# Kernel optimization log

Hardware: AMD Instinct MI355X
Metric: run time of the kernel (lower is better)

The kernel has to match this reference:

```python
import jax, jax.numpy as jnp
import numpy as np
from jax import lax

B, CI, CO, H, W, N, K = 16, 200, 128, 128, 128, 1024, 3
EPS = 1e-5


def setup_inputs() -> dict:
    key = jax.random.key(0)
    ks = jax.random.split(key, 23)
    rn = lambda i, s: jax.random.normal(ks[i], s, jnp.float32)
    ru = lambda i, s: jax.random.uniform(ks[i], s, jnp.float32)
    return {
        "X_in": rn(0, (B, CI, H, W)),
        "H_in": rn(1, (B, CI, N)),
        "bn1_gamma": ru(2, (CI,)),
        "bn1_beta": rn(3, (CI,)) * 0.1,
        "bn1_mean": rn(4, (CI,)) * 0.1,
        "bn1_var": ru(5, (CI,)) + 0.5,
        "bn2_gamma": ru(6, (CI,)),
        "bn2_beta": rn(7, (CI,)) * 0.1,
        "bn2_mean": rn(8, (CI,)) * 0.1,
        "bn2_var": ru(9, (CI,)) + 0.5,
        "W_lin": rn(10, (CO, CI)) * 0.05,
        "b_lin": rn(11, (CO,)) * 0.01,
        "W_sim": rn(12, (CO, CO)) * 0.05,
        "b_sim": rn(13, (CO,)) * 0.01,
        "W_score": rn(14, (CO, CO)) * 0.05,
        "b_score": rn(15, (CO,)) * 0.01,
        "W_dw": rn(16, (CO, 1, K, K)) * 0.1,
        "b_dw": rn(17, (CO,)) * 0.01,
        "W_final": rn(18, (CO, CI + CO)) * 0.05,
        "b_final": rn(19, (CO,)) * 0.01,
        "act_a": ru(20, (1,)),
        "act2_a": ru(21, (1,)),
        "final_a": ru(22, (1,)),
    }


def _bn(x, g, be, m, v):
    # BatchNorm1d eval: x [b,c,n]
    s = g / jnp.sqrt(v + EPS)
    return (x - m[None, :, None]) * s[None, :, None] + be[None, :, None]


def _c1(x, Wt, bi):
    # 1x1 Conv1d: x [b,c,n] -> [b,o,n]
    return jnp.einsum('oc,bcn->bon', Wt, x) + bi[None, :, None]


def _prelu(x, a):
    return jnp.where(x >= 0, x, a * x)


def reference(X_in, H_in, bn1_gamma, bn1_beta, bn1_mean, bn1_var,
              bn2_gamma, bn2_beta, bn2_mean, bn2_var,
              W_lin, b_lin, W_sim, b_sim, W_score, b_score,
              W_dw, b_dw, W_final, b_final, act_a, act2_a, final_a):
    b, c, h, w = X_in.shape
    n = H_in.shape[-1]
    Xr = X_in.reshape(b, c, h * w)
    X_bn = _bn(Xr, bn1_gamma, bn1_beta, bn1_mean, bn1_var)      # [b,ci,hw]
    H_bn = _bn(H_in, bn2_gamma, bn2_beta, bn2_mean, bn2_var)    # [b,ci,n]
    X = _c1(X_bn, W_lin, b_lin)                                  # [b,co,hw]
    Hn = _c1(H_bn, W_lin, b_lin)                                 # [b,co,n]
    X_mean = jnp.mean(X, axis=-1, keepdims=True)                 # [b,co,1]
    X_sim = _c1(X_mean, W_sim, b_sim)                            # [b,co,1]
    H_sim = _c1(Hn, W_sim, b_sim)                                # [b,co,n]
    H_sim2 = jnp.concatenate([X_sim, H_sim], axis=-1)            # [b,co,n+1]
    q = X_sim[:, :, 0]                                           # [b,co]
    sim = jax.nn.sigmoid(jnp.einsum('bc,bcn->bn', q, H_sim2))    # [b,n+1]
    sim = jax.nn.softmax(sim, axis=-1)
    vals = jnp.concatenate([X_mean, Hn], axis=-1)                # [b,co,n+1]
    X_aggre = jnp.einsum('bn,bcn->bc', sim, vals)                # [b,co]
    score = jax.nn.sigmoid(X_aggre @ W_score.T + b_score)        # [b,co]
    X4 = X.reshape(b, -1, h, w)
    Xdw = lax.conv_general_dilated(X4, W_dw, (1, 1), [(K // 2, K // 2)] * 2,
                                   feature_group_count=X4.shape[1],
                                   dimension_numbers=('NCHW', 'OIHW', 'NCHW'))
    Xdw = Xdw + b_dw[None, :, None, None]
    s4 = score[:, :, None, None]
    Xg = s4 * X_aggre[:, :, None, None] + (1.0 - s4) * Xdw       # gated blend
    Xg = _prelu(Xg, act_a)
    Hn = _prelu(Hn, act2_a)
    H_out = _prelu(_c1(jnp.concatenate([Hn, H_bn], axis=1), W_final, b_final), final_a)
    X_out = _prelu(_c1(jnp.concatenate([Xg.reshape(b, -1, h * w), X_bn], axis=1),
                       W_final, b_final), final_a)
    return X_out.reshape(b, -1, h, w), H_out
```

## Files before the change

### kernel.cpp

```cpp
#include <hip/hip_runtime.h>

constexpr int BB = 16;
constexpr int CI = 200;
constexpr int CO = 128;
constexpr int IMG_H = 128;
constexpr int IMG_W = 128;
constexpr int HW = IMG_H * IMG_W;
constexpr int NN = 1024;
constexpr int KT = CO + CI;

constexpr size_t OFF_X      = 0;
constexpr size_t OFF_HN     = (size_t)BB * CO * HW;
constexpr size_t OFF_WLIN1T = OFF_HN + (size_t)BB * CO * NN;
constexpr size_t OFF_WLIN2T = OFF_WLIN1T + (size_t)CI * CO;
constexpr size_t OFF_BLIN1  = OFF_WLIN2T + (size_t)CI * CO;
constexpr size_t OFF_BLIN2  = OFF_BLIN1 + CO;
constexpr size_t OFF_WCXT   = OFF_BLIN2 + CO;
constexpr size_t OFF_WCHT   = OFF_WCXT + (size_t)KT * CO;
constexpr size_t OFF_BFX    = OFF_WCHT + (size_t)KT * CO;
constexpr size_t OFF_BFH    = OFF_BFX + CO;
constexpr size_t OFF_XMSUM  = OFF_BFH + CO;
constexpr size_t OFF_GA     = OFF_XMSUM + (size_t)BB * CO;
constexpr size_t OFF_GB     = OFF_GA + (size_t)BB * CO;

__device__ __forceinline__ float preluf(float v, float a) { return v >= 0.f ? v : a * v; }

#define GEMM_FMA_8x8(wrow, xrow)                                        \
  {                                                                     \
    float4 a0 = *(const float4*)(wrow);                                 \
    float4 a1 = *(const float4*)((wrow) + 4);                           \
    float4 b0 = *(const float4*)(xrow);                                 \
    float4 b1 = *(const float4*)((xrow) + 4);                           \
    float av[8] = {a0.x, a0.y, a0.z, a0.w, a1.x, a1.y, a1.z, a1.w};     \
    float bv[8] = {b0.x, b0.y, b0.z, b0.w, b1.x, b1.y, b1.z, b1.w};     \
    _Pragma("unroll")                                                   \
    for (int ii = 0; ii < 8; ++ii)                                      \
      _Pragma("unroll")                                                 \
      for (int jj = 0; jj < 8; ++jj)                                    \
        acc[ii][jj] = fmaf(av[ii], bv[jj], acc[ii][jj]);                \
  }

__global__ __launch_bounds__(256) void k_prep(
    const float* __restrict__ bn1g, const float* __restrict__ bn1b,
    const float* __restrict__ bn1m, const float* __restrict__ bn1v,
    const float* __restrict__ bn2g, const float* __restrict__ bn2b,
    const float* __restrict__ bn2m, const float* __restrict__ bn2v,
    const float* __restrict__ Wlin, const float* __restrict__ blin,
    const float* __restrict__ Wfin, const float* __restrict__ bfin,
    float* ws)
{
  __shared__ float a1[CI], d1[CI], a2[CI], d2[CI];
  __shared__ float red[256];
  const int o = blockIdx.x;
  const int t = threadIdx.x;
  if (t < CI) {
    float s1 = bn1g[t] * rsqrtf(bn1v[t] + 1e-5f);
    a1[t] = s1; d1[t] = bn1b[t] - bn1m[t] * s1;
    float s2 = bn2g[t] * rsqrtf(bn2v[t] + 1e-5f);
    a2[t] = s2; d2[t] = bn2b[t] - bn2m[t] * s2;
  }
  __syncthreads();
  for (int k = t; k < CI; k += 256) {
    float w = Wlin[o * CI + k];
    ws[OFF_WLIN1T + (size_t)k * CO + o] = w * a1[k];
    ws[OFF_WLIN2T + (size_t)k * CO + o] = w * a2[k];
  }
  for (int k = t; k < KT; k += 256) {
    float w = Wfin[o * KT + k];
    float wx = w, wh = w;
    if (k >= CO) { wx = w * a1[k - CO]; wh = w * a2[k - CO]; }
    ws[OFF_WCXT + (size_t)k * CO + o] = wx;
    ws[OFF_WCHT + (size_t)k * CO + o] = wh;
  }
  if (t < BB) ws[OFF_XMSUM + (size_t)t * CO + o] = 0.f;

  float p1 = 0.f, p2 = 0.f, p3 = 0.f, p4 = 0.f;
  if (t < CI) {
    float wl = Wlin[o * CI + t];
    float wf = Wfin[o * KT + CO + t];
    p1 = wl * d1[t]; p2 = wl * d2[t];
    p3 = wf * d1[t]; p4 = wf * d2[t];
  }
  __syncthreads();
  red[t] = p1; __syncthreads();
  for (int s = 128; s > 0; s >>= 1) { if (t < s) red[t] += red[t + s]; __syncthreads(); }
  if (t == 0) ws[OFF_BLIN1 + o] = blin[o] + red[0];
  __syncthreads();
  red[t] = p2; __syncthreads();
  for (int s = 128; s > 0; s >>= 1) { if (t < s) red[t] += red[t + s]; __syncthreads(); }
  if (t == 0) ws[OFF_BLIN2 + o] = blin[o] + red[0];
  __syncthreads();
  red[t] = p3; __syncthreads();
  for (int s = 128; s > 0; s >>= 1) { if (t < s) red[t] += red[t + s]; __syncthreads(); }
  if (t == 0) ws[OFF_BFX + o] = bfin[o] + red[0];
  __syncthreads();
  red[t] = p4; __syncthreads();
  for (int s = 128; s > 0; s >>= 1) { if (t < s) red[t] += red[t + s]; __syncthreads(); }
  if (t == 0) ws[OFF_BFH + o] = bfin[o] + red[0];
}

__global__ __launch_bounds__(256) void k_hn(const float* __restrict__ Hin, float* ws)
{
  __shared__ __align__(16) float smem[2048];
  float* wt = smem;
  float* xb = smem + 1024;
  const float* WT = ws + OFF_WLIN2T;
  const float* bias = ws + OFF_BLIN2;
  float* Hn = ws + OFF_HN;
  const int bb = blockIdx.y;
  const int col0 = blockIdx.x * 128;
  const int tid = threadIdx.x;
  const int ty = tid >> 4, tx = tid & 15;
  const int kk = tid >> 5, j4 = tid & 31;
  float acc[8][8];
#pragma unroll
  for (int i = 0; i < 8; ++i)
#pragma unroll
    for (int j = 0; j < 8; ++j) acc[i][j] = 0.f;
  const float* Bsrc = Hin + (size_t)bb * CI * NN + col0;
  for (int k0 = 0; k0 < CI; k0 += 8) {
    ((float4*)wt)[tid] = ((const float4*)(WT + (size_t)(k0 + kk) * CO))[j4];
    ((float4*)xb)[tid] = ((const float4*)(Bsrc + (size_t)(k0 + kk) * NN))[j4];
    __syncthreads();
#pragma unroll
    for (int k = 0; k < 8; ++k) {
      const float* wrow = wt + k * 128 + ty * 8;
      const float* xrow = xb + k * 128 + tx * 8;
      GEMM_FMA_8x8(wrow, xrow);
    }
    __syncthreads();
  }
#pragma unroll
  for (int i = 0; i < 8; ++i) {
    const int o = ty * 8 + i;
    const float bi = bias[o];
    float* dst = Hn + ((size_t)(bb * CO + o)) * NN + col0 + tx * 8;
    *(float4*)dst       = make_float4(acc[i][0] + bi, acc[i][1] + bi, acc[i][2] + bi, acc[i][3] + bi);
    *(float4*)(dst + 4) = make_float4(acc[i][4] + bi, acc[i][5] + bi, acc[i][6] + bi, acc[i][7] + bi);
  }
}

__global__ __launch_bounds__(256) void k_x(const float* __restrict__ Xin, float* ws)
{
  __shared__ __align__(16) float smem[2048];
  float* wt = smem;
  float* xb = smem + 1024;
  const float* WT = ws + OFF_WLIN1T;
  const float* bias = ws + OFF_BLIN1;
  float* X = ws + OFF_X;
  const int bb = blockIdx.y;
  const int col0 = blockIdx.x * 128;
  const int tid = threadIdx.x;
  const int ty = tid >> 4, tx = tid & 15;
  const int kk = tid >> 5, j4 = tid & 31;
  float acc[8][8];
#pragma unroll
  for (int i = 0; i < 8; ++i)
#pragma unroll
    for (int j = 0; j < 8; ++j) acc[i][j] = 0.f;
  const float* Bsrc = Xin + (size_t)bb * CI * HW + col0;
  for (int k0 = 0; k0 < CI; k0 += 8) {
    ((float4*)wt)[tid] = ((const float4*)(WT + (size_t)(k0 + kk) * CO))[j4];
    ((float4*)xb)[tid] = ((const float4*)(Bsrc + (size_t)(k0 + kk) * HW))[j4];
    __syncthreads();
#pragma unroll
    for (int k = 0; k < 8; ++k) {
      const float* wrow = wt + k * 128 + ty * 8;
      const float* xrow = xb + k * 128 + tx * 8;
      GEMM_FMA_8x8(wrow, xrow);
    }
    __syncthreads();
  }
  float ps[8];
#pragma unroll
  for (int i = 0; i < 8; ++i) {
    const int o = ty * 8 + i;
    const float bi = bias[o];
    float s = 0.f;
#pragma unroll
    for (int j = 0; j < 8; ++j) s += acc[i][j];
    ps[i] = s;
    float* dst = X + ((size_t)(bb * CO + o)) * HW + col0 + tx * 8;
    *(float4*)dst       = make_float4(acc[i][0] + bi, acc[i][1] + bi, acc[i][2] + bi, acc[i][3] + bi);
    *(float4*)(dst + 4) = make_float4(acc[i][4] + bi, acc[i][5] + bi, acc[i][6] + bi, acc[i][7] + bi);
  }
  __syncthreads();
  float* red = smem;
#pragma unroll
  for (int i = 0; i < 8; ++i) red[(ty * 8 + i) * 16 + tx] = ps[i];
  __syncthreads();
  if (tid < 128) {
    float s = 0.f;
#pragma unroll
    for (int u = 0; u < 16; ++u) s += red[tid * 16 + u];
    atomicAdd(ws + OFF_XMSUM + (size_t)bb * CO + tid, s);
  }
}

__global__ __launch_bounds__(256) void k_small(
    const float* __restrict__ Wsim, const float* __restrict__ bsim,
    const float* __restrict__ Wscore, const float* __restrict__ bscore,
    float* ws)
{
  __shared__ float xmean[128], q[128], u[128], xa[128];
  __shared__ float sim[1025];
  __shared__ float red[256];
  __shared__ float cq_sh, l0_sh, msh, ssh;
  const int bb = blockIdx.x, t = threadIdx.x;
  const float* Hn = ws + OFF_HN + (size_t)bb * CO * NN;
  if (t < 128) xmean[t] = ws[OFF_XMSUM + (size_t)bb * CO + t] * (1.f / 16384.f) + ws[OFF_BLIN1 + t];
  __syncthreads();
  if (t < 128) {
    float s = bsim[t];
    for (int c = 0; c < 128; ++c) s = fmaf(Wsim[t * 128 + c], xmean[c], s);
    q[t] = s;
  }
  __syncthreads();
  if (t < 128) {
    float s = 0.f;
    for (int o = 0; o < 128; ++o) s = fmaf(Wsim[o * 128 + t], q[o], s);
    u[t] = s;
  }
  float pc = 0.f, pl = 0.f;
  if (t < 128) { pc = q[t] * bsim[t]; pl = q[t] * q[t]; }
  red[t] = pc; __syncthreads();
  for (int s = 128; s > 0; s >>= 1) { if (t < s) red[t] += red[t + s]; __syncthreads(); }
  if (t == 0) cq_sh = red[0];
  __syncthreads();
  red[t] = pl; __syncthreads();
  for (int s = 128; s > 0; s >>= 1) { if (t < s) red[t] += red[t + s]; __syncthreads(); }
  if (t == 0) l0_sh = red[0];
  __syncthreads();
  const float cq = cq_sh;
  for (int n = t; n < 1024; n += 256) {
    float s = cq;
    for (int c = 0; c < 128; ++c) s = fmaf(u[c], Hn[(size_t)c * NN + n], s);
    sim[n + 1] = 1.f / (1.f + expf(-s));
  }
  if (t == 0) sim[0] = 1.f / (1.f + expf(-l0_sh));
  __syncthreads();
  float m = -1e30f;
  for (int n = t; n < 1025; n += 256) m = fmaxf(m, sim[n]);
  red[t] = m; __syncthreads();
  for (int s = 128; s > 0; s >>= 1) { if (t < s) red[t] = fmaxf(red[t], red[t + s]); __syncthreads(); }
  if (t == 0) msh = red[0];
  __syncthreads();
  m = msh;
  float pssum = 0.f;
  for (int n = t; n < 1025; n += 256) { float e = expf(sim[n] - m); sim[n] = e; pssum += e; }
  red[t] = pssum; __syncthreads();
  for (int s = 128; s > 0; s >>= 1) { if (t < s) red[t] += red[t + s]; __syncthreads(); }
  if (t == 0) ssh = red[0];
  __syncthreads();
  const float inv = 1.f / ssh;
  {
    const int c = t >> 1, hf = t & 1;
    const float* hr = Hn + (size_t)c * NN + hf * 512;
    const float* sr = sim + 1 + hf * 512;
    float pa = 0.f;
    for (int n = 0; n < 512; ++n) pa = fmaf(sr[n], hr[n], pa);
    red[t] = pa;
  }
  __syncthreads();
  if (t < 128) xa[t] = (red[2 * t] + red[2 * t + 1] + sim[0] * xmean[t]) * inv;
  __syncthreads();
  if (t < 128) {
    float s = bscore[t];
    for (int c = 0; c < 128; ++c) s = fmaf(Wscore[t * 128 + c], xa[c], s);
    float sc = 1.f / (1.f + expf(-s));
    ws[OFF_GA + (size_t)bb * CO + t] = sc * xa[t];
    ws[OFF_GB + (size_t)bb * CO + t] = 1.f - sc;
  }
}

__global__ __launch_bounds__(256) void k_hout(
    const float* __restrict__ Hin, const float* __restrict__ act2_a,
    const float* __restrict__ final_a, float* ws, float* __restrict__ dout)
{
  __shared__ __align__(16) float smem[2048];
  float* wt = smem;
  float* xb = smem + 1024;
  const float* WT = ws + OFF_WCHT;
  const float* bias = ws + OFF_BFH;
  const float* Hn = ws + OFF_HN;
  const int bb = blockIdx.y;
  const int col0 = blockIdx.x * 128;
  const int tid = threadIdx.x;
  const int ty = tid >> 4, tx = tid & 15;
  const int kk = tid >> 5, j4 = tid & 31;
  const float a2 = act2_a[0], fa = final_a[0];
  float acc[8][8];
#pragma unroll
  for (int i = 0; i < 8; ++i)
#pragma unroll
    for (int j = 0; j < 8; ++j) acc[i][j] = 0.f;
  for (int k0 = 0; k0 < KT; k0 += 8) {
    ((float4*)wt)[tid] = ((const float4*)(WT + (size_t)(k0 + kk) * CO))[j4];
    const int krow = k0 + kk;
    float4 v;
    if (krow < CO) {
      v = ((const float4*)(Hn + ((size_t)(bb * CO + krow)) * NN + col0))[j4];
      v.x = preluf(v.x, a2); v.y = preluf(v.y, a2);
      v.z = preluf(v.z, a2); v.w = preluf(v.w, a2);
    } else {
      v = ((const float4*)(Hin + ((size_t)(bb * CI + (krow - CO))) * NN + col0))[j4];
    }
    ((float4*)xb)[tid] = v;
    __syncthreads();
#pragma unroll
    for (int k = 0; k < 8; ++k) {
      const float* wrow = wt + k * 128 + ty * 8;
      const float* xrow = xb + k * 128 + tx * 8;
      GEMM_FMA_8x8(wrow, xrow);
    }
    __syncthreads();
  }
  float* Hout = dout + (size_t)BB * CO * HW;
#pragma unroll
  for (int i = 0; i < 8; ++i) {
    const int o = ty * 8 + i;
    const float bi = bias[o];
    float r[8];
#pragma unroll
    for (int j = 0; j < 8; ++j) r[j] = preluf(acc[i][j] + bi, fa);
    float* dst = Hout + ((size_t)(bb * CO + o)) * NN + col0 + tx * 8;
    *(float4*)dst       = make_float4(r[0], r[1], r[2], r[3]);
    *(float4*)(dst + 4) = make_float4(r[4], r[5], r[6], r[7]);
  }
}

__global__ __launch_bounds__(256) void k_xout(
    const float* __restrict__ Xin, const float* __restrict__ Wdw,
    const float* __restrict__ bdw, const float* __restrict__ act_a,
    const float* __restrict__ final_a, float* ws, float* __restrict__ dout)
{
  __shared__ __align__(16) float xg[128 * 128];
  __shared__ __align__(16) float smem[2048];
  __shared__ float wdw[128 * 9];
  __shared__ float gav[128], gbv[128];
  const int bb = blockIdx.y, y = blockIdx.x, tid = threadIdx.x;
  const float* Xw = ws + OFF_X;
  const float aa = act_a[0], fa = final_a[0];
  for (int i = tid; i < 128 * 9; i += 256) wdw[i] = Wdw[i];
  if (tid < 128) {
    gav[tid] = ws[OFF_GA + (size_t)bb * CO + tid];
    gbv[tid] = ws[OFF_GB + (size_t)bb * CO + tid];
  }
  __syncthreads();
  {
    const int px = tid & 127, half = tid >> 7;
    for (int c = half; c < CO; c += 2) {
      const float* base = Xw + ((size_t)(bb * CO + c)) * HW + y * IMG_W;
      const float* wc = wdw + c * 9;
      float v = bdw[c];
#pragma unroll
      for (int dy = -1; dy <= 1; ++dy) {
        const int yy = y + dy;
        if (yy < 0 || yy >= IMG_H) continue;
        const float* row = base + dy * IMG_W;
#pragma unroll
        for (int dx = -1; dx <= 1; ++dx) {
          const int xx = px + dx;
          if (xx < 0 || xx >= IMG_W) continue;
          v = fmaf(row[xx], wc[(dy + 1) * 3 + (dx + 1)], v);
        }
      }
      float g = gav[c] + gbv[c] * v;
      xg[c * 128 + px] = preluf(g, aa);
    }
  }
  __syncthreads();
  float* wt = smem;
  float* xb = smem + 1024;
  const float* WT = ws + OFF_WCXT;
  const float* bias = ws + OFF_BFX;
  const int ty = tid >> 4, tx = tid & 15;
  const int kk = tid >> 5, j4 = tid & 31;
  float acc[8][8];
#pragma unroll
  for (int i = 0; i < 8; ++i)
#pragma unroll
    for (int j = 0; j < 8; ++j) acc[i][j] = 0.f;
  for (int k0 = 0; k0 < KT; k0 += 8) {
    ((float4*)wt)[tid] = ((const float4*)(WT + (size_t)(k0 + kk) * CO))[j4];
    const bool fromX = (k0 >= CO);
    if (fromX) {
      ((float4*)xb)[tid] =
          ((const float4*)(Xin + ((size_t)(bb * CI + (k0 + kk - CO))) * HW + y * IMG_W))[j4];
    }
    __syncthreads();
    const float* bbase = fromX ? xb : (xg + k0 * 128);
#pragma unroll
    for (int k = 0; k < 8; ++k) {
      const float* wrow = wt + k * 128 + ty * 8;
      const float* xrow = bbase + k * 128 + tx * 8;
      GEMM_FMA_8x8(wrow, xrow);
    }
    __syncthreads();
  }
#pragma unroll
  for (int i = 0; i < 8; ++i) {
    const int o = ty * 8 + i;
    const float bi = bias[o];
    float r[8];
#pragma unroll
    for (int j = 0; j < 8; ++j) r[j] = preluf(acc[i][j] + bi, fa);
    float* dst = dout + ((size_t)(bb * CO + o)) * HW + y * IMG_W + tx * 8;
    *(float4*)dst       = make_float4(r[0], r[1], r[2], r[3]);
    *(float4*)(dst + 4) = make_float4(r[4], r[5], r[6], r[7]);
  }
}

extern "C" void kernel_launch(void* const* d_in, const int* in_sizes, int n_in,
                              void* d_out, int out_size, void* d_ws, size_t ws_size,
                              hipStream_t stream)
{
  const float* Xin   = (const float*)d_in[0];
  const float* Hin   = (const float*)d_in[1];
  const float* bn1g  = (const float*)d_in[2];
  const float* bn1b  = (const float*)d_in[3];
  const float* bn1m  = (const float*)d_in[4];
  const float* bn1v  = (const float*)d_in[5];
  const float* bn2g  = (const float*)d_in[6];
  const float* bn2b  = (const float*)d_in[7];
  const float* bn2m  = (const float*)d_in[8];
  const float* bn2v  = (const float*)d_in[9];
  const float* Wlin  = (const float*)d_in[10];
  const float* blin  = (const float*)d_in[11];
  const float* Wsim  = (const float*)d_in[12];
  const float* bsim  = (const float*)d_in[13];
  const float* Wscr  = (const float*)d_in[14];
  const float* bscr  = (const float*)d_in[15];
  const float* Wdw   = (const float*)d_in[16];
  const float* bdw   = (const float*)d_in[17];
  const float* Wfin  = (const float*)d_in[18];
  const float* bfin  = (const float*)d_in[19];
  const float* acta  = (const float*)d_in[20];
  const float* act2a = (const float*)d_in[21];
  const float* fina  = (const float*)d_in[22];
  float* ws  = (float*)d_ws;
  float* out = (float*)d_out;

  k_prep<<<dim3(128), dim3(256), 0, stream>>>(bn1g, bn1b, bn1m, bn1v,
                                              bn2g, bn2b, bn2m, bn2v,
                                              Wlin, blin, Wfin, bfin, ws);
  k_hn<<<dim3(8, 16), dim3(256), 0, stream>>>(Hin, ws);
  k_x<<<dim3(128, 16), dim3(256), 0, stream>>>(Xin, ws);
  k_small<<<dim3(16), dim3(256), 0, stream>>>(Wsim, bsim, Wscr, bscr, ws);
  k_hout<<<dim3(8, 16), dim3(256), 0, stream>>>(Hin, act2a, fina, ws, out);
  k_xout<<<dim3(128, 16), dim3(256), 0, stream>>>(Xin, Wdw, bdw, acta, fina, ws, out);
}
```

Measured before the change: 1.300 ms.

## Use bf16 MFMA for the X projection and store intermediate X as bf16

Replaces the fp32 FMA GEMM that computes X from the batch-normed input with a bf16 MFMA kernel (16x16x32) that uses swizzled LDS tiles, register-prefetched global loads and padded K. The intermediate X is stored as bf16, which halves its write and read traffic in the depthwise conv stage. The final X output GEMM keeps fp32 weights but stages its activations as bf16 in LDS and prefetches the next tile into registers. The cost is reduced precision in X, the gated blend and the final GEMM inputs, which may raise numerical error.

New measurement: 1.137 ms. -12.5%, faster.

```diff
diff --git a/kernel.cpp b/kernel.cpp
--- a/kernel.cpp
+++ b/kernel.cpp
@@ -8,22 +8,37 @@
 constexpr int HW = IMG_H * IMG_W;
 constexpr int NN = 1024;
 constexpr int KT = CO + CI;
-
-constexpr size_t OFF_X      = 0;
-constexpr size_t OFF_HN     = (size_t)BB * CO * HW;
-constexpr size_t OFF_WLIN1T = OFF_HN + (size_t)BB * CO * NN;
-constexpr size_t OFF_WLIN2T = OFF_WLIN1T + (size_t)CI * CO;
-constexpr size_t OFF_BLIN1  = OFF_WLIN2T + (size_t)CI * CO;
-constexpr size_t OFF_BLIN2  = OFF_BLIN1 + CO;
-constexpr size_t OFF_WCXT   = OFF_BLIN2 + CO;
-constexpr size_t OFF_WCHT   = OFF_WCXT + (size_t)KT * CO;
-constexpr size_t OFF_BFX    = OFF_WCHT + (size_t)KT * CO;
-constexpr size_t OFF_BFH    = OFF_BFX + CO;
-constexpr size_t OFF_XMSUM  = OFF_BFH + CO;
-constexpr size_t OFF_GA     = OFF_XMSUM + (size_t)BB * CO;
-constexpr size_t OFF_GB     = OFF_GA + (size_t)BB * CO;
+constexpr int KP = 224;
+
+constexpr size_t F_XBF    = 0;
+constexpr size_t F_HN     = 16777216;
+constexpr size_t F_WLIN1T = F_HN + 2097152;
+constexpr size_t F_WLIN2T = F_WLIN1T + 25600;
+constexpr size_t F_BLIN1  = F_WLIN2T + 25600;
+constexpr size_t F_BLIN2  = F_BLIN1 + 128;
+constexpr size_t F_WCXT   = F_BLIN2 + 128;
+constexpr size_t F_WCHT   = F_WCXT + 41984;
+constexpr size_t F_BFX    = F_WCHT + 41984;
+constexpr size_t F_BFH    = F_BFX + 128;
+constexpr size_t F_XMSUM  = F_BFH + 128;
+constexpr size_t F_GA     = F_XMSUM + 2048;
+constexpr size_t F_GB     = F_GA + 2048;
+constexpr size_t F_WB1    = F_GB + 2048;
+constexpr size_t F_END    = F_WB1 + 14336;
+
+typedef __attribute__((ext_vector_type(8))) short short8v;
+typedef __attribute__((ext_vector_type(4))) float f32x4;
 
 __device__ __forceinline__ float preluf(float v, float a) { return v >= 0.f ? v : a * v; }
+__device__ __forceinline__ ushort f2bf(float f) {
+  union { float f; unsigned u; } x; x.f = f;
+  unsigned r = (x.u + 0x7FFFu + ((x.u >> 16) & 1u)) >> 16;
+  return (ushort)r;
+}
+__device__ __forceinline__ float bf2f(ushort u) {
+  union { unsigned u; float f; } x; x.u = ((unsigned)u) << 16;
+  return x.f;
+}
 
 #define GEMM_FMA_8x8(wrow, xrow)                                        \
   {                                                                     \
@@ -40,6 +55,23 @@
         acc[ii][jj] = fmaf(av[ii], bv[jj], acc[ii][jj]);                \
   }
 
+#define GEMM_FMA_8x8_BF(wrow, xrowu)                                    \
+  {                                                                     \
+    float4 a0 = *(const float4*)(wrow);                                 \
+    float4 a1 = *(const float4*)((wrow) + 4);                           \
+    uint4 bu = *(const uint4*)(xrowu);                                  \
+    float av[8] = {a0.x, a0.y, a0.z, a0.w, a1.x, a1.y, a1.z, a1.w};     \
+    float bv[8] = {bf2f((ushort)(bu.x & 0xffff)), bf2f((ushort)(bu.x >> 16)), \
+                   bf2f((ushort)(bu.y & 0xffff)), bf2f((ushort)(bu.y >> 16)), \
+                   bf2f((ushort)(bu.z & 0xffff)), bf2f((ushort)(bu.z >> 16)), \
+                   bf2f((ushort)(bu.w & 0xffff)), bf2f((ushort)(bu.w >> 16))}; \
+    _Pragma("unroll")                                                   \
+    for (int ii = 0; ii < 8; ++ii)                                      \
+      _Pragma("unroll")                                                 \
+      for (int jj = 0; jj < 8; ++jj)                                    \
+        acc[ii][jj] = fmaf(av[ii], bv[jj], acc[ii][jj]);                \
+  }
+
 __global__ __launch_bounds__(256) void k_prep(
     const float* __restrict__ bn1g, const float* __restrict__ bn1b,
     const float* __restrict__ bn1m, const float* __restrict__ bn1v,
@@ -47,7 +79,11 @@
     const float* __restrict__ bn2m, const float* __restrict__ bn2v,
     const float* __restrict__ Wlin, const float* __restrict__ blin,
     const float* __restrict__ Wfin, const float* __restrict__ bfin,
-    float* ws)
+    float* __restrict__ wlin1t, float* __restrict__ wlin2t,
+    float* __restrict__ blin1, float* __restrict__ blin2,
+    float* __restrict__ wcxt, float* __restrict__ wcht,
+    float* __restrict__ bfx, float* __restrict__ bfh,
+    float* __restrict__ xmsum, ushort* __restrict__ wb1)
 {
   __shared__ float a1[CI], d1[CI], a2[CI], d2[CI];
   __shared__ float red[256];
@@ -60,19 +96,23 @@
     a2[t] = s2; d2[t] = bn2b[t] - bn2m[t] * s2;
   }
   __syncthreads();
-  for (int k = t; k < CI; k += 256) {
-    float w = Wlin[o * CI + k];
-    ws[OFF_WLIN1T + (size_t)k * CO + o] = w * a1[k];
-    ws[OFF_WLIN2T + (size_t)k * CO + o] = w * a2[k];
+  if (t < CI) {
+    float w = Wlin[o * CI + t];
+    wlin1t[(size_t)t * CO + o] = w * a1[t];
+    wlin2t[(size_t)t * CO + o] = w * a2[t];
+  }
+  if (t < KP) {
+    float v = (t < CI) ? Wlin[o * CI + t] * a1[t] : 0.f;
+    wb1[o * KP + t] = f2bf(v);
   }
   for (int k = t; k < KT; k += 256) {
     float w = Wfin[o * KT + k];
     float wx = w, wh = w;
     if (k >= CO) { wx = w * a1[k - CO]; wh = w * a2[k - CO]; }
-    ws[OFF_WCXT + (size_t)k * CO + o] = wx;
-    ws[OFF_WCHT + (size_t)k * CO + o] = wh;
-  }
-  if (t < BB) ws[OFF_XMSUM + (size_t)t * CO + o] = 0.f;
+    wcxt[(size_t)k * CO + o] = wx;
+    wcht[(size_t)k * CO + o] = wh;
+  }
+  if (t < BB) xmsum[(size_t)t * CO + o] = 0.f;
 
   float p1 = 0.f, p2 = 0.f, p3 = 0.f, p4 = 0.f;
   if (t < CI) {
@@ -84,29 +124,149 @@
   __syncthreads();
   red[t] = p1; __syncthreads();
   for (int s = 128; s > 0; s >>= 1) { if (t < s) red[t] += red[t + s]; __syncthreads(); }
-  if (t == 0) ws[OFF_BLIN1 + o] = blin[o] + red[0];
+  if (t == 0) blin1[o] = blin[o] + red[0];
   __syncthreads();
   red[t] = p2; __syncthreads();
   for (int s = 128; s > 0; s >>= 1) { if (t < s) red[t] += red[t + s]; __syncthreads(); }
-  if (t == 0) ws[OFF_BLIN2 + o] = blin[o] + red[0];
+  if (t == 0) blin2[o] = blin[o] + red[0];
   __syncthreads();
   red[t] = p3; __syncthreads();
   for (int s = 128; s > 0; s >>= 1) { if (t < s) red[t] += red[t + s]; __syncthreads(); }
-  if (t == 0) ws[OFF_BFX + o] = bfin[o] + red[0];
+  if (t == 0) bfx[o] = bfin[o] + red[0];
   __syncthreads();
   red[t] = p4; __syncthreads();
   for (int s = 128; s > 0; s >>= 1) { if (t < s) red[t] += red[t + s]; __syncthreads(); }
-  if (t == 0) ws[OFF_BFH + o] = bfin[o] + red[0];
-}
-
-__global__ __launch_bounds__(256) void k_hn(const float* __restrict__ Hin, float* ws)
+  if (t == 0) bfh[o] = bfin[o] + red[0];
+}
+
+__global__ __launch_bounds__(256) void k_x_mfma(
+    const float* __restrict__ Xin, const ushort* __restrict__ Wb,
+    const float* __restrict__ bias, ushort* __restrict__ XBF,
+    float* __restrict__ xmsum)
+{
+  __shared__ __align__(16) ushort lds[8192];
+  const int b = blockIdx.y;
+  const int n0 = blockIdx.x * 128;
+  const int tid = threadIdx.x;
+  const int l = tid & 63, w = tid >> 6;
+  const int wr = w >> 1, wc = w & 1;
+  const int g = l >> 4, r15 = l & 15;
+
+  int aoff[2];
+  size_t agl[2];
+#pragma unroll
+  for (int r = 0; r < 2; ++r) {
+    int id = r * 256 + tid;
+    int row = id >> 2, cs = id & 3;
+    int cd = cs ^ ((row >> 1) & 3);
+    aoff[r] = row * 32 + cs * 8;
+    agl[r] = (size_t)row * KP + cd * 8;
+  }
+  const int nB = tid & 127, khB = tid >> 7;
+  const int sB = (nB >> 1) & 3;
+  const int bw0 = 4096 + nB * 32 + (((2 * khB)     ^ sB) * 8);
+  const int bw1 = 4096 + nB * 32 + (((2 * khB + 1) ^ sB) * 8);
+  const float* bsrc = Xin + (size_t)b * CI * HW + n0 + nB;
+
+  int aidx[4], bidx[4];
+#pragma unroll
+  for (int mi = 0; mi < 4; ++mi) {
+    int o = wr * 64 + mi * 16 + r15;
+    aidx[mi] = o * 32 + ((g ^ ((o >> 1) & 3)) * 8);
+  }
+#pragma unroll
+  for (int ni = 0; ni < 4; ++ni) {
+    int n = wc * 64 + ni * 16 + r15;
+    bidx[ni] = 4096 + n * 32 + ((g ^ ((n >> 1) & 3)) * 8);
+  }
+
+  f32x4 acc[4][4];
+#pragma unroll
+  for (int mi = 0; mi < 4; ++mi)
+#pragma unroll
+    for (int ni = 0; ni < 4; ++ni) acc[mi][ni] = (f32x4)(0.f);
+
+  uint4 areg0 = *(const uint4*)(Wb + agl[0]);
+  uint4 areg1 = *(const uint4*)(Wb + agl[1]);
+  float bregs[16];
+#pragma unroll
+  for (int j = 0; j < 16; ++j) {
+    const int k = khB * 16 + j;
+    bregs[j] = bsrc[(size_t)k * HW];
+  }
+
+  for (int ks = 0; ks < 7; ++ks) {
+    *(uint4*)(lds + aoff[0]) = areg0;
+    *(uint4*)(lds + aoff[1]) = areg1;
+    unsigned pk[8];
+#pragma unroll
+    for (int q = 0; q < 8; ++q)
+      pk[q] = (unsigned)f2bf(bregs[2 * q]) | ((unsigned)f2bf(bregs[2 * q + 1]) << 16);
+    *(uint4*)(lds + bw0) = make_uint4(pk[0], pk[1], pk[2], pk[3]);
+    *(uint4*)(lds + bw1) = make_uint4(pk[4], pk[5], pk[6], pk[7]);
+    __syncthreads();
+    if (ks < 6) {
+      const size_t ko = (size_t)(ks + 1) * 32;
+      areg0 = *(const uint4*)(Wb + agl[0] + ko);
+      areg1 = *(const uint4*)(Wb + agl[1] + ko);
+#pragma unroll
+      for (int j = 0; j < 16; ++j) {
+        const int k = (ks + 1) * 32 + khB * 16 + j;
+        bregs[j] = (k < CI) ? bsrc[(size_t)k * HW] : 0.f;
+      }
+    }
+    short8v av[4], bv[4];
+#pragma unroll
+    for (int mi = 0; mi < 4; ++mi) av[mi] = *(const short8v*)(lds + aidx[mi]);
+#pragma unroll
+    for (int ni = 0; ni < 4; ++ni) bv[ni] = *(const short8v*)(lds + bidx[ni]);
+#pragma unroll
+    for (int mi = 0; mi < 4; ++mi)
+#pragma unroll
+      for (int ni = 0; ni < 4; ++ni)
+        acc[mi][ni] = __builtin_amdgcn_mfma_f32_16x16x32_bf16(av[mi], bv[ni], acc[mi][ni], 0, 0, 0);
+    __syncthreads();
+  }
+
+#pragma unroll
+  for (int mi = 0; mi < 4; ++mi)
+#pragma unroll
+    for (int e = 0; e < 4; ++e) {
+      const int o = wr * 64 + mi * 16 + g * 4 + e;
+      const float bi = bias[o];
+      const size_t rowbase = ((size_t)(b * CO + o)) * HW + n0;
+#pragma unroll
+      for (int ni = 0; ni < 4; ++ni) {
+        const int n = wc * 64 + ni * 16 + r15;
+        XBF[rowbase + n] = f2bf(acc[mi][ni][e] + bi);
+      }
+    }
+  float* red = (float*)lds;
+#pragma unroll
+  for (int mi = 0; mi < 4; ++mi)
+#pragma unroll
+    for (int e = 0; e < 4; ++e) {
+      const int o = wr * 64 + mi * 16 + g * 4 + e;
+      float s = acc[mi][0][e] + acc[mi][1][e] + acc[mi][2][e] + acc[mi][3][e];
+      red[o * 32 + wc * 16 + r15] = s;
+    }
+  __syncthreads();
+  if (tid < 128) {
+    float s = 0.f;
+#pragma unroll
+    for (int j = 0; j < 32; ++j) s += red[tid * 32 + j];
+    atomicAdd(xmsum + (size_t)b * CO + tid, s);
+  }
+}
+
+__global__ __launch_bounds__(256) void k_hn(const float* __restrict__ Hin,
+                                            const float* __restrict__ WT,
+                                            const float* __restrict__ bias,
+                                            float* __restrict__ Hn)
 {
   __shared__ __align__(16) float smem[2048];
   float* wt = smem;
   float* xb = smem + 1024;
-  const float* WT = ws + OFF_WLIN2T;
-  const float* bias = ws + OFF_BLIN2;
-  float* Hn = ws + OFF_HN;
   const int bb = blockIdx.y;
   const int col0 = blockIdx.x * 128;
   const int tid = threadIdx.x;
@@ -140,75 +300,20 @@
   }
 }
 
-__global__ __launch_bounds__(256) void k_x(const float* __restrict__ Xin, float* ws)
-{
-  __shared__ __align__(16) float smem[2048];
-  float* wt = smem;
-  float* xb = smem + 1024;
-  const float* WT = ws + OFF_WLIN1T;
-  const float* bias = ws + OFF_BLIN1;
-  float* X = ws + OFF_X;
-  const int bb = blockIdx.y;
-  const int col0 = blockIdx.x * 128;
-  const int tid = threadIdx.x;
-  const int ty = tid >> 4, tx = tid & 15;
-  const int kk = tid >> 5, j4 = tid & 31;
-  float acc[8][8];
-#pragma unroll
-  for (int i = 0; i < 8; ++i)
-#pragma unroll
-    for (int j = 0; j < 8; ++j) acc[i][j] = 0.f;
-  const float* Bsrc = Xin + (size_t)bb * CI * HW + col0;
-  for (int k0 = 0; k0 < CI; k0 += 8) {
-    ((float4*)wt)[tid] = ((const float4*)(WT + (size_t)(k0 + kk) * CO))[j4];
-    ((float4*)xb)[tid] = ((const float4*)(Bsrc + (size_t)(k0 + kk) * HW))[j4];
-    __syncthreads();
-#pragma unroll
-    for (int k = 0; k < 8; ++k) {
-      const float* wrow = wt + k * 128 + ty * 8;
-      const float* xrow = xb + k * 128 + tx * 8;
-      GEMM_FMA_8x8(wrow, xrow);
-    }
-    __syncthreads();
-  }
-  float ps[8];
-#pragma unroll
-  for (int i = 0; i < 8; ++i) {
-    const int o = ty * 8 + i;
-    const float bi = bias[o];
-    float s = 0.f;
-#pragma unroll
-    for (int j = 0; j < 8; ++j) s += acc[i][j];
-    ps[i] = s;
-    float* dst = X + ((size_t)(bb * CO + o)) * HW + col0 + tx * 8;
-    *(float4*)dst       = make_float4(acc[i][0] + bi, acc[i][1] + bi, acc[i][2] + bi, acc[i][3] + bi);
-    *(float4*)(dst + 4) = make_float4(acc[i][4] + bi, acc[i][5] + bi, acc[i][6] + bi, acc[i][7] + bi);
-  }
-  __syncthreads();
-  float* red = smem;
-#pragma unroll
-  for (int i = 0; i < 8; ++i) red[(ty * 8 + i) * 16 + tx] = ps[i];
-  __syncthreads();
-  if (tid < 128) {
-    float s = 0.f;
-#pragma unroll
-    for (int u = 0; u < 16; ++u) s += red[tid * 16 + u];
-    atomicAdd(ws + OFF_XMSUM + (size_t)bb * CO + tid, s);
-  }
-}
-
 __global__ __launch_bounds__(256) void k_small(
     const float* __restrict__ Wsim, const float* __restrict__ bsim,
     const float* __restrict__ Wscore, const float* __restrict__ bscore,
-    float* ws)
+    const float* __restrict__ HnG, const float* __restrict__ xmsum,
+    const float* __restrict__ blin1, float* __restrict__ ga,
+    float* __restrict__ gb)
 {
   __shared__ float xmean[128], q[128], u[128], xa[128];
   __shared__ float sim[1025];
   __shared__ float red[256];
   __shared__ float cq_sh, l0_sh, msh, ssh;
   const int bb = blockIdx.x, t = threadIdx.x;
-  const float* Hn = ws + OFF_HN + (size_t)bb * CO * NN;
-  if (t < 128) xmean[t] = ws[OFF_XMSUM + (size_t)bb * CO + t] * (1.f / 16384.f) + ws[OFF_BLIN1 + t];
+  const float* Hn = HnG + (size_t)bb * CO * NN;
+  if (t < 128) xmean[t] = xmsum[(size_t)bb * CO + t] * (1.f / 16384.f) + blin1[t];
   __syncthreads();
   if (t < 128) {
     float s = bsim[t];
@@ -268,21 +373,20 @@
     float s = bscore[t];
     for (int c = 0; c < 128; ++c) s = fmaf(Wscore[t * 128 + c], xa[c], s);
     float sc = 1.f / (1.f + expf(-s));
-    ws[OFF_GA + (size_t)bb * CO + t] = sc * xa[t];
-    ws[OFF_GB + (size_t)bb * CO + t] = 1.f - sc;
+    ga[(size_t)bb * CO + t] = sc * xa[t];
+    gb[(size_t)bb * CO + t] = 1.f - sc;
   }
 }
 
 __global__ __launch_bounds__(256) void k_hout(
     const float* __restrict__ Hin, const float* __restrict__ act2_a,
-    const float* __restrict__ final_a, float* ws, float* __restrict__ dout)
+    const float* __restrict__ final_a, const float* __restrict__ WT,
+    const float* __restrict__ bias, const float* __restrict__ HnG,
+    float* __restrict__ dout)
 {
   __shared__ __align__(16) float smem[2048];
   float* wt = smem;
   float* xb = smem + 1024;
-  const float* WT = ws + OFF_WCHT;
-  const float* bias = ws + OFF_BFH;
-  const float* Hn = ws + OFF_HN;
   const int bb = blockIdx.y;
   const int col0 = blockIdx.x * 128;
   const int tid = threadIdx.x;
@@ -299,7 +403,7 @@
     const int krow = k0 + kk;
     float4 v;
     if (krow < CO) {
-      v = ((const float4*)(Hn + ((size_t)(bb * CO + krow)) * NN + col0))[j4];
+      v = ((const float4*)(HnG + ((size_t)(bb * CO + krow)) * NN + col0))[j4];
       v.x = preluf(v.x, a2); v.y = preluf(v.y, a2);
       v.z = preluf(v.z, a2); v.w = preluf(v.w, a2);
     } else {
@@ -330,78 +434,86 @@
 }
 
 __global__ __launch_bounds__(256) void k_xout(
-    const float* __restrict__ Xin, const float* __restrict__ Wdw,
-    const float* __restrict__ bdw, const float* __restrict__ act_a,
-    const float* __restrict__ final_a, float* ws, float* __restrict__ dout)
-{
-  __shared__ __align__(16) float xg[128 * 128];
-  __shared__ __align__(16) float smem[2048];
-  __shared__ float wdw[128 * 9];
+    const float* __restrict__ Xin, const ushort* __restrict__ XBF,
+    const float* __restrict__ Wdw, const float* __restrict__ bdw,
+    const float* __restrict__ act_a, const float* __restrict__ final_a,
+    const float* __restrict__ wcxt, const float* __restrict__ bfx,
+    const float* __restrict__ ga, const float* __restrict__ gb,
+    float* __restrict__ dout)
+{
+  __shared__ __align__(16) ushort xg[128 * 128];
+  __shared__ __align__(16) float wt[1024];
+  __shared__ __align__(16) ushort xb[1024];
+  __shared__ float wdw[1152];
   __shared__ float gav[128], gbv[128];
   const int bb = blockIdx.y, y = blockIdx.x, tid = threadIdx.x;
-  const float* Xw = ws + OFF_X;
   const float aa = act_a[0], fa = final_a[0];
-  for (int i = tid; i < 128 * 9; i += 256) wdw[i] = Wdw[i];
+  for (int i = tid; i < 1152; i += 256) wdw[i] = Wdw[i];
   if (tid < 128) {
-    gav[tid] = ws[OFF_GA + (size_t)bb * CO + tid];
-    gbv[tid] = ws[OFF_GB + (size_t)bb * CO + tid];
+    gav[tid] = ga[(size_t)bb * CO + tid];
+    gbv[tid] = gb[(size_t)bb * CO + tid];
   }
   __syncthreads();
   {
     const int px = tid & 127, half = tid >> 7;
     for (int c = half; c < CO; c += 2) {
-      const float* base = Xw + ((size_t)(bb * CO + c)) * HW + y * IMG_W;
+      const ushort* base = XBF + ((size_t)(bb * CO + c)) * HW + y * IMG_W;
       const float* wc = wdw + c * 9;
       float v = bdw[c];
 #pragma unroll
       for (int dy = -1; dy <= 1; ++dy) {
         const int yy = y + dy;
         if (yy < 0 || yy >= IMG_H) continue;
-        const float* row = base + dy * IMG_W;
+        const ushort* row = base + dy * IMG_W;
 #pragma unroll
         for (int dx = -1; dx <= 1; ++dx) {
           const int xx = px + dx;
           if (xx < 0 || xx >= IMG_W) continue;
-          v = fmaf(row[xx], wc[(dy + 1) * 3 + (dx + 1)], v);
+          v = fmaf(bf2f(row[xx]), wc[(dy + 1) * 3 + (dx + 1)], v);
         }
       }
-      float g = gav[c] + gbv[c] * v;
-      xg[c * 128 + px] = preluf(g, aa);
-    }
-  }
-  __syncthreads();
-  float* wt = smem;
-  float* xb = smem + 1024;
-  const float* WT = ws + OFF_WCXT;
-  const float* bias = ws + OFF_BFX;
+      float gv = gav[c] + gbv[c] * v;
+      xg[c * 128 + px] = f2bf(preluf(gv, aa));
+    }
+  }
+  __syncthreads();
   const int ty = tid >> 4, tx = tid & 15;
-  const int kk = tid >> 5, j4 = tid & 31;
+  const int kk8 = tid >> 5, j4 = tid & 31;
   float acc[8][8];
 #pragma unroll
   for (int i = 0; i < 8; ++i)
 #pragma unroll
     for (int j = 0; j < 8; ++j) acc[i][j] = 0.f;
+  float4 wreg = ((const float4*)(wcxt + (size_t)kk8 * CO))[j4];
+  float4 xreg = make_float4(0.f, 0.f, 0.f, 0.f);
   for (int k0 = 0; k0 < KT; k0 += 8) {
-    ((float4*)wt)[tid] = ((const float4*)(WT + (size_t)(k0 + kk) * CO))[j4];
+    ((float4*)wt)[tid] = wreg;
     const bool fromX = (k0 >= CO);
     if (fromX) {
-      ((float4*)xb)[tid] =
-          ((const float4*)(Xin + ((size_t)(bb * CI + (k0 + kk - CO))) * HW + y * IMG_W))[j4];
-    }
-    __syncthreads();
-    const float* bbase = fromX ? xb : (xg + k0 * 128);
+      uint2 p;
+      p.x = (unsigned)f2bf(xreg.x) | ((unsigned)f2bf(xreg.y) << 16);
+      p.y = (unsigned)f2bf(xreg.z) | ((unsigned)f2bf(xreg.w) << 16);
+      ((uint2*)xb)[tid] = p;
+    }
+    __syncthreads();
+    if (k0 + 8 < KT) {
+      wreg = ((const float4*)(wcxt + (size_t)(k0 + 8 + kk8) * CO))[j4];
+      if (k0 + 8 >= CO)
+        xreg = ((const float4*)(Xin + ((size_t)(bb * CI + (k0 + 8 + kk8 - CO))) * HW + y * IMG_W))[j4];
+    }
+    const ushort* bbase = fromX ? xb : (xg + k0 * 128);
 #pragma unroll
     for (int k = 0; k < 8; ++k) {
       const float* wrow = wt + k * 128 + ty * 8;
-      const float* xrow = bbase + k * 128 + tx * 8;
-      GEMM_FMA_8x8(wrow, xrow);
+      const ushort* xrow = bbase + k * 128 + tx * 8;
+      GEMM_FMA_8x8_BF(wrow, xrow);
     }
     __syncthreads();
   }
 #pragma unroll
   for (int i = 0; i < 8; ++i) {
     const int o = ty * 8 + i;
-    const float bi = bias[o];
+    const float bi = bfx[o];
     float r[8];
 #pragma unroll
     for (int j = 0; j < 8; ++j) r[j] = preluf(acc[i][j] + bi, fa);
@@ -438,15 +550,31 @@
   const float* acta  = (const float*)d_in[20];
   const float* act2a = (const float*)d_in[21];
   const float* fina  = (const float*)d_in[22];
-  float* ws  = (float*)d_ws;
+  float* wsf = (float*)d_ws;
   float* out = (float*)d_out;
 
-  k_prep<<<dim3(128), dim3(256), 0, stream>>>(bn1g, bn1b, bn1m, bn1v,
-                                              bn2g, bn2b, bn2m, bn2v,
-                                              Wlin, blin, Wfin, bfin, ws);
-  k_hn<<<dim3(8, 16), dim3(256), 0, stream>>>(Hin, ws);
-  k_x<<<dim3(128, 16), dim3(256), 0, stream>>>(Xin, ws);
-  k_small<<<dim3(16), dim3(256), 0, stream>>>(Wsim, bsim, Wscr, bscr, ws);
-  k_hout<<<dim3(8, 16), dim3(256), 0, stream>>>(Hin, act2a, fina, ws, out);
-  k_xout<<<dim3(128, 16), dim3(256), 0, stream>>>(Xin, Wdw, bdw, acta, fina, ws, out);
-}
+  ushort* XBF   = (ushort*)d_ws;
+  float*  HN    = wsf + F_HN;
+  float*  WL1T  = wsf + F_WLIN1T;
+  float*  WL2T  = wsf + F_WLIN2T;
+  float*  BL1   = wsf + F_BLIN1;
+  float*  BL2   = wsf + F_BLIN2;
+  float*  WCXTp = wsf + F_WCXT;
+  float*  WCHTp = wsf + F_WCHT;
+  float*  BFXp  = wsf + F_BFX;
+  float*  BFHp  = wsf + F_BFH;
+  float*  XMS   = wsf + F_XMSUM;
+  float*  GAp   = wsf + F_GA;
+  float*  GBp   = wsf + F_GB;
+  ushort* WB1   = (ushort*)(wsf + F_WB1);
+
+  k_prep<<<dim3(128), dim3(256), 0, stream>>>(
+      bn1g, bn1b, bn1m, bn1v, bn2g, bn2b, bn2m, bn2v, Wlin, blin, Wfin, bfin,
+      WL1T, WL2T, BL1, BL2, WCXTp, WCHTp, BFXp, BFHp, XMS, WB1);
+  k_hn<<<dim3(8, 16), dim3(256), 0, stream>>>(Hin, WL2T, BL2, HN);
+  k_x_mfma<<<dim3(128, 16), dim3(256), 0, stream>>>(Xin, WB1, BL1, XBF, XMS);
+  k_small<<<dim3(16), dim3(256), 0, stream>>>(Wsim, bsim, Wscr, bscr, HN, XMS, BL1, GAp, GBp);
+  k_hout<<<dim3(8, 16), dim3(256), 0, stream>>>(Hin, act2a, fina, WCHTp, BFHp, HN, out);
+  k_xout<<<dim3(128, 16), dim3(256), 0, stream>>>(Xin, XBF, Wdw, bdw, acta, fina,
+                                                  WCXTp, BFXp, GAp, GBp, out);
+}
```
